# Performance work log

Hardware: AMD Instinct MI355X
Metric: run time of the kernel (lower is better)

The kernel has to match this reference:

```python
import jax, jax.numpy as jnp
import numpy as np

B, F, V, D_EMB = 16384, 32, 50000, 16
D_IN = F * D_EMB            # 512, concat embedding dim
N_TASK, N_SPEC, N_SH = 2, 2, 2
E = N_TASK * N_SPEC + N_SH  # 6 experts per CGC level
H1, H2 = 512, 256           # expert_params dims
T1, T2 = 128, 64            # tower dims


def setup_inputs() -> dict:
    key = jax.random.key(0)
    ks = iter(jax.random.split(key, 32))
    def w(shape, s=0.05):
        return jax.random.normal(next(ks), shape, jnp.float32) * s
    return dict(
        x_ids=jax.random.randint(next(ks), (B, F), 0, V),
        emb=w((F, V, D_EMB)),
        e1_W1=w((E, D_IN, H1)), e1_b1=jnp.zeros((E, H1), jnp.float32),
        e1_W2=w((E, H1, H2)), e1_b2=jnp.zeros((E, H2), jnp.float32),
        g1_Ws=w((N_TASK, D_IN, N_SPEC + N_SH)), g1_bs=jnp.zeros((N_TASK, N_SPEC + N_SH), jnp.float32),
        g1_Wsh=w((D_IN, E)), g1_bsh=jnp.zeros((E,), jnp.float32),
        e2_W1=w((E, H2, H1)), e2_b1=jnp.zeros((E, H1), jnp.float32),
        e2_W2=w((E, H1, H2)), e2_b2=jnp.zeros((E, H2), jnp.float32),
        g2_Ws=w((N_TASK, H2, N_SPEC + N_SH)), g2_bs=jnp.zeros((N_TASK, N_SPEC + N_SH), jnp.float32),
        tw_W1=w((N_TASK, H2, T1)), tw_b1=jnp.zeros((N_TASK, T1), jnp.float32),
        tw_W2=w((N_TASK, T1, T2)), tw_b2=jnp.zeros((N_TASK, T2), jnp.float32),
    )


def _cgc(x_list, W1, b1, W2, b2, Wg, bg, Wg_sh=None, bg_sh=None):
    # Stack expert inputs: task-t specific experts read x_list[t], shared read x_list[-1].
    X = jnp.stack([x_list[0]] * N_SPEC + [x_list[1]] * N_SPEC + [x_list[-1]] * N_SH)  # [E,B,Din]
    # Grouped two-layer expert MLP (BatchNorm is identity at eval-mode init).
    h = jax.nn.relu(jnp.einsum('ebd,edh->ebh', X, W1) + b1[:, None, :])   # [E,B,H1]
    out = jax.nn.relu(jnp.einsum('ebh,eho->ebo', h, W2) + b2[:, None, :])  # [E,B,H2]
    outs = []
    for t in range(N_TASK):
        gate = jax.nn.softmax(x_list[t] @ Wg[t] + bg[t], axis=-1)          # [B, N_SPEC+N_SH]
        sel = jnp.concatenate([out[t * N_SPEC:(t + 1) * N_SPEC], out[-N_SH:]], axis=0)
        outs.append(jnp.einsum('bk,kbo->bo', gate, sel))
    if Wg_sh is not None:  # shared gate only for levels < n_level
        gate = jax.nn.softmax(x_list[-1] @ Wg_sh + bg_sh, axis=-1)          # [B,E]
        outs.append(jnp.einsum('bk,kbo->bo', gate, out))
    return outs


def reference(x_ids, emb, e1_W1, e1_b1, e1_W2, e1_b2, g1_Ws, g1_bs, g1_Wsh, g1_bsh,
              e2_W1, e2_b1, e2_W2, e2_b2, g2_Ws, g2_bs, tw_W1, tw_b1, tw_W2, tw_b2):
    # Embedding lookup per sparse feature, then flatten (squeeze_dim=True).
    embed_x = emb[jnp.arange(F)[None, :], x_ids].reshape(B, D_IN)  # [B, 512]
    xs = [embed_x] * (N_TASK + 1)
    xs = _cgc(xs, e1_W1, e1_b1, e1_W2, e1_b2, g1_Ws, g1_bs, g1_Wsh, g1_bsh)  # level 1 -> 3 outs
    xs = _cgc(xs, e2_W1, e2_b1, e2_W2, e2_b2, g2_Ws, g2_bs)                  # level 2 -> 2 outs
    ys = []
    for t in range(N_TASK):
        h = jax.nn.relu(xs[t] @ tw_W1[t] + tw_b1[t])
        h = jax.nn.relu(h @ tw_W2[t] + tw_b2[t])
        ys.append(jax.nn.sigmoid(h))  # PredictionLayer('classification')
    return jnp.concatenate(ys, axis=1)  # [B, N_TASK*T2]
```

## Files before the change

### kernel.cpp

```cpp
#include <hip/hip_runtime.h>

typedef unsigned short u16;
typedef __attribute__((ext_vector_type(4))) unsigned short u16x4;
typedef __attribute__((ext_vector_type(8))) unsigned short u16x8;
typedef __attribute__((ext_vector_type(8))) short s16x8;
typedef __attribute__((ext_vector_type(4))) float f32x4;

#define BATCH 16384
#define NFEAT 32
#define NVOCAB 50000

__device__ __forceinline__ u16 f2bf(float f) {
    union { float f; unsigned u; } v; v.f = f;
    unsigned u = v.u;
    return (u16)((u + 0x7fffu + ((u >> 16) & 1u)) >> 16);
}
__device__ __forceinline__ float bf2f(u16 h) {
    union { unsigned u; float f; } v; v.u = ((unsigned)h) << 16;
    return v.f;
}

__device__ __forceinline__ void load_lds16(const u16* g, u16* l) {
    __builtin_amdgcn_global_load_lds(
        (const __attribute__((address_space(1))) void*)g,
        (__attribute__((address_space(3))) void*)l, 16, 0, 0);
}

struct PrepDesc { const float* src; u16* dst; int K; int N; int nz; int zbase; };
struct PrepArgs { PrepDesc d[6]; };

__global__ void prep_weights(PrepArgs args) {
    int z = blockIdx.z;
    int di = 0;
    #pragma unroll
    for (int i = 0; i < 6; i++)
        if (z >= args.d[i].zbase && z < args.d[i].zbase + args.d[i].nz) di = i;
    PrepDesc d = args.d[di];
    int zz = z - d.zbase;
    int k0 = blockIdx.x * 32, n0 = blockIdx.y * 32;
    if (k0 >= d.K || n0 >= d.N) return;
    __shared__ float tile[32][33];
    const float* src = d.src + (long)zz * d.K * d.N;
    u16* dst = d.dst + (long)zz * d.K * d.N;
    int tx = threadIdx.x & 31, ty = threadIdx.x >> 5;
    for (int r = ty; r < 32; r += 8) {
        int k = k0 + r, n = n0 + tx;
        tile[r][tx] = (k < d.K && n < d.N) ? src[(long)k * d.N + n] : 0.f;
    }
    __syncthreads();
    for (int r = ty; r < 32; r += 8) {
        int n = n0 + r, k = k0 + tx;
        if (n < d.N && k < d.K) dst[(long)n * d.K + k] = f2bf(tile[tx][r]);
    }
}

__global__ void gather_embed(const int* __restrict__ ids,
                             const float* __restrict__ emb,
                             u16* __restrict__ out) {
    int idx = blockIdx.x * 256 + threadIdx.x;
    int d4 = idx & 3;
    int f  = (idx >> 2) & 31;
    int b  = idx >> 7;
    int id = ids[b * NFEAT + f];
    const float4* p = (const float4*)(emb + ((long)f * NVOCAB + id) * 16) + d4;
    float4 v = *p;
    u16x4 o;
    o.x = f2bf(v.x); o.y = f2bf(v.y); o.z = f2bf(v.z); o.w = f2bf(v.w);
    *(u16x4*)(out + (long)b * 512 + f * 16 + d4 * 4) = o;
}

struct GemmP {
    const u16* A; const u16* Bt; const float* bias; u16* C;
    int N, K, a_zshift, c_row_stride; long a_zstride, c_zstride;
};

__device__ __forceinline__ void gemm_impl(const GemmP p) {
    __shared__ u16 sA[128 * 64];
    __shared__ u16 sB[256 * 64];
    const int z = blockIdx.z;
    const u16* Ab = p.A + (long)(z >> p.a_zshift) * p.a_zstride;
    const u16* Bb = p.Bt + (long)z * p.N * p.K;
    const int m0 = blockIdx.x * 128;
    const int n0 = blockIdx.y * 256;
    const int tid = threadIdx.x;
    const int lane = tid & 63;
    const int w = tid >> 6;
    const int wm = (w & 1) * 64;
    const int wn = (w >> 1) * 128;
    const int l16 = lane & 15;
    const int q = lane >> 4;
    const int key = l16 & 7;
    const int K = p.K;

    const int tr = tid >> 3;
    const int lc = (tid & 7) ^ (tr & 7);
    const u16* gA0 = Ab + (long)(m0 + tr) * K + lc * 8;
    const u16* gB0 = Bb + (long)(n0 + tr) * K + lc * 8;
    u16* lA0 = &sA[(tid & ~63) * 8];
    u16* lB0 = &sB[(tid & ~63) * 8];

    f32x4 acc[4][8] = {};

    for (int k0 = 0; k0 < K; k0 += 64) {
        if (k0) __syncthreads();
        #pragma unroll
        for (int i = 0; i < 4; i++)
            load_lds16(gA0 + (long)(32 * i) * K + k0, lA0 + i * 256 * 8);
        #pragma unroll
        for (int i = 0; i < 8; i++)
            load_lds16(gB0 + (long)(32 * i) * K + k0, lB0 + i * 256 * 8);
        __syncthreads();
        #pragma unroll
        for (int kk = 0; kk < 2; kk++) {
            const int pc = ((kk << 2) | q) ^ key;
            s16x8 af[4], bf[8];
            #pragma unroll
            for (int mt = 0; mt < 4; mt++)
                af[mt] = *(const s16x8*)(&sA[(wm + mt * 16 + l16) * 64 + pc * 8]);
            #pragma unroll
            for (int nt = 0; nt < 8; nt++)
                bf[nt] = *(const s16x8*)(&sB[(wn + nt * 16 + l16) * 64 + pc * 8]);
            #pragma unroll
            for (int mt = 0; mt < 4; mt++)
                #pragma unroll
                for (int nt = 0; nt < 8; nt++)
                    acc[mt][nt] = __builtin_amdgcn_mfma_f32_16x16x32_bf16(
                        bf[nt], af[mt], acc[mt][nt], 0, 0, 0);
        }
    }

    const float* bb = p.bias + (long)z * p.N;
    u16* Cp = p.C + (long)z * p.c_zstride;
    #pragma unroll
    for (int mt = 0; mt < 4; mt++) {
        int grow = m0 + wm + mt * 16 + l16;
        u16* rowp = Cp + (long)grow * p.c_row_stride;
        #pragma unroll
        for (int nt = 0; nt < 8; nt++) {
            int gc = n0 + wn + nt * 16 + q * 4;
            float4 bv = *(const float4*)(bb + gc);
            f32x4 v = acc[mt][nt];
            v.x = fmaxf(v.x + bv.x, 0.f);
            v.y = fmaxf(v.y + bv.y, 0.f);
            v.z = fmaxf(v.z + bv.z, 0.f);
            v.w = fmaxf(v.w + bv.w, 0.f);
            u16x4 o;
            o.x = f2bf(v.x); o.y = f2bf(v.y); o.z = f2bf(v.z); o.w = f2bf(v.w);
            *(u16x4*)(rowp + gc) = o;
        }
    }
}

__global__ __launch_bounds__(256, 2) void gemm_l1a(GemmP p) { gemm_impl(p); }
__global__ __launch_bounds__(256, 2) void gemm_l1b(GemmP p) { gemm_impl(p); }
__global__ __launch_bounds__(256, 2) void gemm_l2a(GemmP p) { gemm_impl(p); }
__global__ __launch_bounds__(256, 2) void gemm_l2b(GemmP p) { gemm_impl(p); }

__global__ __launch_bounds__(256, 1)
void tower_fused(const u16* __restrict__ x2, const u16* __restrict__ W1t,
                 const float* __restrict__ b1, const u16* __restrict__ W2t,
                 const float* __restrict__ b2, float* __restrict__ out) {
    const int t = blockIdx.y, m0 = blockIdx.x * 64;
    __shared__ u16 sX[64 * 256];
    __shared__ u16 sW1[128 * 256];
    __shared__ u16 sH[64 * 136];
    __shared__ u16 sW2[64 * 128];
    __shared__ float sB1[128];
    __shared__ float sB2[64];
    const int tid = threadIdx.x, lane = tid & 63, w = tid >> 6;
    const int l16 = lane & 15, q = lane >> 4;

    #pragma unroll
    for (int i = 0; i < 8; i++) {
        int c = i * 256 + tid, row = c >> 5, kc = c & 31;
        int lcc = (kc & ~7) | ((kc & 7) ^ (row & 7));
        load_lds16(x2 + ((long)t * BATCH + m0 + row) * 256 + lcc * 8,
                   &sX[(i * 256 + (tid & ~63)) * 8]);
    }
    #pragma unroll
    for (int i = 0; i < 16; i++) {
        int c = i * 256 + tid, row = c >> 5, kc = c & 31;
        int lcc = (kc & ~7) | ((kc & 7) ^ (row & 7));
        load_lds16(W1t + ((long)t * 128 + row) * 256 + lcc * 8,
                   &sW1[(i * 256 + (tid & ~63)) * 8]);
    }
    #pragma unroll
    for (int i = 0; i < 4; i++) {
        int c = i * 256 + tid, row = c >> 4, kc = c & 15;
        int lcc = (kc & ~7) | ((kc & 7) ^ (row & 7));
        load_lds16(W2t + ((long)t * 64 + row) * 128 + lcc * 8,
                   &sW2[(i * 256 + (tid & ~63)) * 8]);
    }
    if (tid < 128) sB1[tid] = b1[t * 128 + tid];
    if (tid < 64)  sB2[tid] = b2[t * 64 + tid];
    __syncthreads();

    f32x4 acc1[4][2] = {};
    #pragma unroll
    for (int kk = 0; kk < 8; kk++) {
        int pcb = kk * 4 + q;
        s16x8 af[4], bf[2];
        #pragma unroll
        for (int mt = 0; mt < 4; mt++) {
            int row = mt * 16 + l16;
            int sc = (pcb & ~7) | ((pcb & 7) ^ (row & 7));
            af[mt] = *(const s16x8*)(&sX[row * 256 + sc * 8]);
        }
        #pragma unroll
        for (int nt = 0; nt < 2; nt++) {
            int row = w * 32 + nt * 16 + l16;
            int sc = (pcb & ~7) | ((pcb & 7) ^ (row & 7));
            bf[nt] = *(const s16x8*)(&sW1[row * 256 + sc * 8]);
        }
        #pragma unroll
        for (int mt = 0; mt < 4; mt++)
            #pragma unroll
            for (int nt = 0; nt < 2; nt++)
                acc1[mt][nt] = __builtin_amdgcn_mfma_f32_16x16x32_bf16(
                    bf[nt], af[mt], acc1[mt][nt], 0, 0, 0);
    }
    #pragma unroll
    for (int mt = 0; mt < 4; mt++) {
        int row = mt * 16 + l16;
        #pragma unroll
        for (int nt = 0; nt < 2; nt++) {
            int col = w * 32 + nt * 16 + q * 4;
            f32x4 v = acc1[mt][nt];
            u16x4 o;
            o.x = f2bf(fmaxf(v.x + sB1[col + 0], 0.f));
            o.y = f2bf(fmaxf(v.y + sB1[col + 1], 0.f));
            o.z = f2bf(fmaxf(v.z + sB1[col + 2], 0.f));
            o.w = f2bf(fmaxf(v.w + sB1[col + 3], 0.f));
            *(u16x4*)(&sH[row * 136 + col]) = o;
        }
    }
    __syncthreads();

    f32x4 acc2[4] = {};
    #pragma unroll
    for (int kk = 0; kk < 4; kk++) {
        s16x8 af[4], bf;
        #pragma unroll
        for (int mt = 0; mt < 4; mt++) {
            int row = mt * 16 + l16;
            af[mt] = *(const s16x8*)(&sH[row * 136 + kk * 32 + q * 8]);
        }
        {
            int row = w * 16 + l16;
            int pc = kk * 4 + q;
            int sc = (pc & ~7) | ((pc & 7) ^ (row & 7));
            bf = *(const s16x8*)(&sW2[row * 128 + sc * 8]);
        }
        #pragma unroll
        for (int mt = 0; mt < 4; mt++)
            acc2[mt] = __builtin_amdgcn_mfma_f32_16x16x32_bf16(
                bf, af[mt], acc2[mt], 0, 0, 0);
    }
    #pragma unroll
    for (int mt = 0; mt < 4; mt++) {
        int grow = m0 + mt * 16 + l16;
        int col = w * 16 + q * 4;
        float4 bv = *(const float4*)(sB2 + col);
        f32x4 v = acc2[mt];
        float4 r;
        r.x = 1.f / (1.f + __expf(-(v.x + bv.x)));
        r.y = 1.f / (1.f + __expf(-(v.y + bv.y)));
        r.z = 1.f / (1.f + __expf(-(v.z + bv.z)));
        r.w = 1.f / (1.f + __expf(-(v.w + bv.w)));
        *(float4*)(out + (long)grow * 128 + t * 64 + col) = r;
    }
}

__global__ __launch_bounds__(256)
void gate1(const u16* __restrict__ embed, const u16* __restrict__ out1,
           const float* __restrict__ g1Ws, const float* __restrict__ g1bs,
           const float* __restrict__ gWsh, const float* __restrict__ gbsh,
           u16* __restrict__ x1) {
    const int m0 = blockIdx.x * 8;
    __shared__ float sg[8][16];
    const int tid = threadIdx.x;
    const int row = tid >> 5, l = tid & 31;
    const long rb = m0 + row;

    float a[4] = {0,0,0,0}, b[4] = {0,0,0,0}, c[6] = {0,0,0,0,0,0};
    {
        const u16* er = embed + rb * 512 + l * 16;
        u16x8 xa = *(const u16x8*)(er);
        u16x8 xb = *(const u16x8*)(er + 8);
        #pragma unroll
        for (int u = 0; u < 16; u++) {
            int k = l * 16 + u;
            float xv = bf2f(u < 8 ? xa[u] : xb[u - 8]);
            float4 wa = *(const float4*)(g1Ws + k * 4);
            float4 wb = *(const float4*)(g1Ws + 2048 + k * 4);
            a[0] += xv * wa.x; a[1] += xv * wa.y; a[2] += xv * wa.z; a[3] += xv * wa.w;
            b[0] += xv * wb.x; b[1] += xv * wb.y; b[2] += xv * wb.z; b[3] += xv * wb.w;
            float2 w0 = *(const float2*)(gWsh + k * 6);
            float2 w1 = *(const float2*)(gWsh + k * 6 + 2);
            float2 w2 = *(const float2*)(gWsh + k * 6 + 4);
            c[0] += xv * w0.x; c[1] += xv * w0.y;
            c[2] += xv * w1.x; c[3] += xv * w1.y;
            c[4] += xv * w2.x; c[5] += xv * w2.y;
        }
    }
    #pragma unroll
    for (int off = 1; off < 32; off <<= 1) {
        #pragma unroll
        for (int g = 0; g < 4; g++) { a[g] += __shfl_xor(a[g], off); b[g] += __shfl_xor(b[g], off); }
        #pragma unroll
        for (int g = 0; g < 6; g++) c[g] += __shfl_xor(c[g], off);
    }
    if (l == 0) {
        float mx, s, e[6];
        mx = -1e30f;
        for (int g = 0; g < 4; g++) { a[g] += g1bs[g]; mx = fmaxf(mx, a[g]); }
        s = 0.f; for (int g = 0; g < 4; g++) { e[g] = __expf(a[g] - mx); s += e[g]; }
        for (int g = 0; g < 4; g++) sg[row][g] = e[g] / s;
        mx = -1e30f;
        for (int g = 0; g < 4; g++) { b[g] += g1bs[4 + g]; mx = fmaxf(mx, b[g]); }
        s = 0.f; for (int g = 0; g < 4; g++) { e[g] = __expf(b[g] - mx); s += e[g]; }
        for (int g = 0; g < 4; g++) sg[row][4 + g] = e[g] / s;
        mx = -1e30f;
        for (int g = 0; g < 6; g++) { c[g] += gbsh[g]; mx = fmaxf(mx, c[g]); }
        s = 0.f; for (int g = 0; g < 6; g++) { e[g] = __expf(c[g] - mx); s += e[g]; }
        for (int g = 0; g < 6; g++) sg[row][8 + g] = e[g] / s;
    }
    __syncthreads();

    const int c8 = l * 8;
    const u16* ob = out1 + rb * 256 + c8;
    u16x8 o[6];
    #pragma unroll
    for (int k = 0; k < 6; k++) o[k] = *(const u16x8*)(ob + (long)k * BATCH * 256);
    const float* g = sg[row];
    u16x8 r0, r1, r2;
    #pragma unroll
    for (int u = 0; u < 8; u++) {
        float o0 = bf2f(o[0][u]), o1 = bf2f(o[1][u]), o2 = bf2f(o[2][u]);
        float o3 = bf2f(o[3][u]), o4 = bf2f(o[4][u]), o5 = bf2f(o[5][u]);
        r0[u] = f2bf(g[0] * o0 + g[1] * o1 + g[2] * o4 + g[3] * o5);
        r1[u] = f2bf(g[4] * o2 + g[5] * o3 + g[6] * o4 + g[7] * o5);
        r2[u] = f2bf(g[8] * o0 + g[9] * o1 + g[10] * o2 + g[11] * o3 + g[12] * o4 + g[13] * o5);
    }
    *(u16x8*)(x1 + ((long)0 * BATCH + rb) * 256 + c8) = r0;
    *(u16x8*)(x1 + ((long)1 * BATCH + rb) * 256 + c8) = r1;
    *(u16x8*)(x1 + ((long)2 * BATCH + rb) * 256 + c8) = r2;
}

__global__ __launch_bounds__(256)
void gate2(const u16* __restrict__ x1, const u16* __restrict__ out2,
           const float* __restrict__ g2Ws, const float* __restrict__ g2bs,
           u16* __restrict__ x2) {
    const int m0 = blockIdx.x * 8;
    __shared__ float sg[8][8];
    const int tid = threadIdx.x;
    const int row = tid >> 5, l = tid & 31;
    const long rb = m0 + row;

    float a[4] = {0,0,0,0}, b[4] = {0,0,0,0};
    {
        const u16* e0 = x1 + rb * 256 + l * 8;
        const u16* e1 = e0 + (long)BATCH * 256;
        u16x8 x0 = *(const u16x8*)e0;
        u16x8 x1v = *(const u16x8*)e1;
        #pragma unroll
        for (int u = 0; u < 8; u++) {
            int k = l * 8 + u;
            float4 wa = *(const float4*)(g2Ws + k * 4);
            float4 wb = *(const float4*)(g2Ws + 1024 + k * 4);
            float xv0 = bf2f(x0[u]), xv1 = bf2f(x1v[u]);
            a[0] += xv0 * wa.x; a[1] += xv0 * wa.y; a[2] += xv0 * wa.z; a[3] += xv0 * wa.w;
            b[0] += xv1 * wb.x; b[1] += xv1 * wb.y; b[2] += xv1 * wb.z; b[3] += xv1 * wb.w;
        }
    }
    #pragma unroll
    for (int off = 1; off < 32; off <<= 1) {
        #pragma unroll
        for (int g = 0; g < 4; g++) { a[g] += __shfl_xor(a[g], off); b[g] += __shfl_xor(b[g], off); }
    }
    if (l == 0) {
        float mx, s, e[4];
        mx = -1e30f;
        for (int g = 0; g < 4; g++) { a[g] += g2bs[g]; mx = fmaxf(mx, a[g]); }
        s = 0.f; for (int g = 0; g < 4; g++) { e[g] = __expf(a[g] - mx); s += e[g]; }
        for (int g = 0; g < 4; g++) sg[row][g] = e[g] / s;
        mx = -1e30f;
        for (int g = 0; g < 4; g++) { b[g] += g2bs[4 + g]; mx = fmaxf(mx, b[g]); }
        s = 0.f; for (int g = 0; g < 4; g++) { e[g] = __expf(b[g] - mx); s += e[g]; }
        for (int g = 0; g < 4; g++) sg[row][4 + g] = e[g] / s;
    }
    __syncthreads();

    const int c8 = l * 8;
    const u16* ob = out2 + rb * 256 + c8;
    u16x8 o[6];
    #pragma unroll
    for (int k = 0; k < 6; k++) o[k] = *(const u16x8*)(ob + (long)k * BATCH * 256);
    const float* g = sg[row];
    u16x8 r0, r1;
    #pragma unroll
    for (int u = 0; u < 8; u++) {
        float o0 = bf2f(o[0][u]), o1 = bf2f(o[1][u]), o2 = bf2f(o[2][u]);
        float o3 = bf2f(o[3][u]), o4 = bf2f(o[4][u]), o5 = bf2f(o[5][u]);
        r0[u] = f2bf(g[0] * o0 + g[1] * o1 + g[2] * o4 + g[3] * o5);
        r1[u] = f2bf(g[4] * o2 + g[5] * o3 + g[6] * o4 + g[7] * o5);
    }
    *(u16x8*)(x2 + ((long)0 * BATCH + rb) * 256 + c8) = r0;
    *(u16x8*)(x2 + ((long)1 * BATCH + rb) * 256 + c8) = r1;
}

extern "C" void kernel_launch(void* const* d_in, const int* in_sizes, int n_in,
                              void* d_out, int out_size, void* d_ws, size_t ws_size,
                              hipStream_t stream) {
    const int*   x_ids = (const int*)  d_in[0];
    const float* emb   = (const float*)d_in[1];
    const float* e1W1  = (const float*)d_in[2];
    const float* e1b1  = (const float*)d_in[3];
    const float* e1W2  = (const float*)d_in[4];
    const float* e1b2  = (const float*)d_in[5];
    const float* g1Ws  = (const float*)d_in[6];
    const float* g1bs  = (const float*)d_in[7];
    const float* g1Wsh = (const float*)d_in[8];
    const float* g1bsh = (const float*)d_in[9];
    const float* e2W1  = (const float*)d_in[10];
    const float* e2b1  = (const float*)d_in[11];
    const float* e2W2  = (const float*)d_in[12];
    const float* e2b2  = (const float*)d_in[13];
    const float* g2Ws  = (const float*)d_in[14];
    const float* g2bs  = (const float*)d_in[15];
    const float* twW1  = (const float*)d_in[16];
    const float* twb1  = (const float*)d_in[17];
    const float* twW2  = (const float*)d_in[18];
    const float* twb2  = (const float*)d_in[19];
    float* out = (float*)d_out;

    char* ws = (char*)d_ws;
    u16* embed   = (u16*)(ws + 0);
    u16* wt_e1W1 = (u16*)(ws + 16777216);
    u16* wt_e1W2 = (u16*)(ws + 19922944);
    u16* wt_e2W1 = (u16*)(ws + 21495808);
    u16* wt_e2W2 = (u16*)(ws + 23068672);
    u16* wt_twW1 = (u16*)(ws + 24641536);
    u16* wt_twW2 = (u16*)(ws + 24772608);
    u16* h_buf   = (u16*)(ws + 24805376);
    u16* o_buf   = (u16*)(ws + 125468672);
    u16* x1      = (u16*)(ws + 175800320);
    u16* x2      = (u16*)(ws + 200966144);

    PrepArgs pa;
    pa.d[0] = { e1W1, wt_e1W1, 512, 512, 6,  0 };
    pa.d[1] = { e1W2, wt_e1W2, 512, 256, 6,  6 };
    pa.d[2] = { e2W1, wt_e2W1, 256, 512, 6, 12 };
    pa.d[3] = { e2W2, wt_e2W2, 512, 256, 6, 18 };
    pa.d[4] = { twW1, wt_twW1, 256, 128, 2, 24 };
    pa.d[5] = { twW2, wt_twW2, 128,  64, 2, 26 };
    prep_weights<<<dim3(16, 16, 28), 256, 0, stream>>>(pa);

    gather_embed<<<dim3(BATCH * NFEAT * 4 / 256), 256, 0, stream>>>(x_ids, emb, embed);

    GemmP p1a = { embed, wt_e1W1, e1b1, h_buf, 512, 512, 0, 512, 0L, (long)BATCH * 512 };
    gemm_l1a<<<dim3(128, 2, 6), 256, 0, stream>>>(p1a);

    GemmP p1b = { h_buf, wt_e1W2, e1b2, o_buf, 256, 512, 0, 256,
                  (long)BATCH * 512, (long)BATCH * 256 };
    gemm_l1b<<<dim3(128, 1, 6), 256, 0, stream>>>(p1b);

    gate1<<<dim3(BATCH / 8), 256, 0, stream>>>(embed, o_buf, g1Ws, g1bs, g1Wsh, g1bsh, x1);

    GemmP p2a = { x1, wt_e2W1, e2b1, h_buf, 512, 256, 1, 512,
                  (long)BATCH * 256, (long)BATCH * 512 };
    gemm_l2a<<<dim3(128, 2, 6), 256, 0, stream>>>(p2a);

    GemmP p2b = { h_buf, wt_e2W2, e2b2, o_buf, 256, 512, 0, 256,
                  (long)BATCH * 512, (long)BATCH * 256 };
    gemm_l2b<<<dim3(128, 1, 6), 256, 0, stream>>>(p2b);

    gate2<<<dim3(BATCH / 8), 256, 0, stream>>>(x1, o_buf, g2Ws, g2bs, x2);

    tower_fused<<<dim3(BATCH / 64, 2), 256, 0, stream>>>(x2, wt_twW1, twb1, wt_twW2, twb2, out);
}
```

Baseline: 522.7 us.

## Fuse all stages into one persistent kernel with software grid barriers

Replaces the nine separate kernel launches (weight prep, gather, four GEMMs, two gates, tower) with a single persistent kernel of 512 blocks. The stages are separated by an atomic-counter grid barrier, and GEMM tiles are distributed round-robin over the blocks. Weight prep and the embedding gather now run concurrently on disjoint block subsets. This is meant to remove per-launch overhead and inter-kernel gaps, at the cost of barrier spin time and a fixed block count that depends on every block being co-resident. The tower now reads weights from global memory instead of staging them in LDS.

```diff
diff --git a/kernel.cpp b/kernel.cpp
--- a/kernel.cpp
+++ b/kernel.cpp
@@ -9,6 +9,7 @@
 #define BATCH 16384
 #define NFEAT 32
 #define NVOCAB 50000
+#define NBLK 512
 
 __device__ __forceinline__ u16 f2bf(float f) {
     union { float f; unsigned u; } v; v.f = f;
@@ -19,69 +20,51 @@
     union { unsigned u; float f; } v; v.u = ((unsigned)h) << 16;
     return v.f;
 }
-
 __device__ __forceinline__ void load_lds16(const u16* g, u16* l) {
     __builtin_amdgcn_global_load_lds(
         (const __attribute__((address_space(1))) void*)g,
         (__attribute__((address_space(3))) void*)l, 16, 0, 0);
 }
 
-struct PrepDesc { const float* src; u16* dst; int K; int N; int nz; int zbase; };
-struct PrepArgs { PrepDesc d[6]; };
-
-__global__ void prep_weights(PrepArgs args) {
-    int z = blockIdx.z;
-    int di = 0;
-    #pragma unroll
-    for (int i = 0; i < 6; i++)
-        if (z >= args.d[i].zbase && z < args.d[i].zbase + args.d[i].nz) di = i;
-    PrepDesc d = args.d[di];
-    int zz = z - d.zbase;
-    int k0 = blockIdx.x * 32, n0 = blockIdx.y * 32;
-    if (k0 >= d.K || n0 >= d.N) return;
-    __shared__ float tile[32][33];
-    const float* src = d.src + (long)zz * d.K * d.N;
-    u16* dst = d.dst + (long)zz * d.K * d.N;
-    int tx = threadIdx.x & 31, ty = threadIdx.x >> 5;
-    for (int r = ty; r < 32; r += 8) {
-        int k = k0 + r, n = n0 + tx;
-        tile[r][tx] = (k < d.K && n < d.N) ? src[(long)k * d.N + n] : 0.f;
-    }
+__device__ __forceinline__ void grid_sync(unsigned* cnt, unsigned* gen) {
     __syncthreads();
-    for (int r = ty; r < 32; r += 8) {
-        int n = n0 + r, k = k0 + tx;
-        if (n < d.N && k < d.K) dst[(long)n * d.K + k] = f2bf(tile[tx][r]);
-    }
-}
-
-__global__ void gather_embed(const int* __restrict__ ids,
-                             const float* __restrict__ emb,
-                             u16* __restrict__ out) {
-    int idx = blockIdx.x * 256 + threadIdx.x;
-    int d4 = idx & 3;
-    int f  = (idx >> 2) & 31;
-    int b  = idx >> 7;
-    int id = ids[b * NFEAT + f];
-    const float4* p = (const float4*)(emb + ((long)f * NVOCAB + id) * 16) + d4;
-    float4 v = *p;
-    u16x4 o;
-    o.x = f2bf(v.x); o.y = f2bf(v.y); o.z = f2bf(v.z); o.w = f2bf(v.w);
-    *(u16x4*)(out + (long)b * 512 + f * 16 + d4 * 4) = o;
-}
-
-struct GemmP {
-    const u16* A; const u16* Bt; const float* bias; u16* C;
-    int N, K, a_zshift, c_row_stride; long a_zstride, c_zstride;
+    if (threadIdx.x == 0) {
+        __threadfence();
+        unsigned arrival = __hip_atomic_fetch_add(cnt, 1u, __ATOMIC_ACQ_REL,
+                                                  __HIP_MEMORY_SCOPE_AGENT) + 1u;
+        unsigned target = (arrival + NBLK - 1u) / NBLK;
+        if (arrival % NBLK == 0u)
+            __hip_atomic_fetch_add(gen, 1u, __ATOMIC_ACQ_REL,
+                                   __HIP_MEMORY_SCOPE_AGENT);
+        while (__hip_atomic_load(gen, __ATOMIC_ACQUIRE,
+                                 __HIP_MEMORY_SCOPE_AGENT) < target)
+            __builtin_amdgcn_s_sleep(1);
+        __threadfence();
+    }
+    __syncthreads();
+}
+
+struct MonoArgs {
+    const int* x_ids; const float* emb;
+    const float* e1W1; const float* e1b1; const float* e1W2; const float* e1b2;
+    const float* g1Ws; const float* g1bs; const float* g1Wsh; const float* g1bsh;
+    const float* e2W1; const float* e2b1; const float* e2W2; const float* e2b2;
+    const float* g2Ws; const float* g2bs;
+    const float* twW1; const float* twb1; const float* twW2; const float* twb2;
+    u16* embed; u16* wt_e1W1; u16* wt_e1W2; u16* wt_e2W1; u16* wt_e2W2;
+    u16* wt_twW1; u16* wt_twW2; u16* h_buf; u16* o_buf; u16* x1; u16* x2;
+    unsigned* bar;
+    float* out;
 };
 
-__device__ __forceinline__ void gemm_impl(const GemmP p) {
-    __shared__ u16 sA[128 * 64];
-    __shared__ u16 sB[256 * 64];
-    const int z = blockIdx.z;
-    const u16* Ab = p.A + (long)(z >> p.a_zshift) * p.a_zstride;
-    const u16* Bb = p.Bt + (long)z * p.N * p.K;
-    const int m0 = blockIdx.x * 128;
-    const int n0 = blockIdx.y * 256;
+__device__ __forceinline__ void gemm_core(const u16* __restrict__ Ab,
+                                          const u16* __restrict__ Bb,
+                                          const float* __restrict__ bb,
+                                          u16* __restrict__ Cp,
+                                          int N, int K, int m0, int n0,
+                                          char* smem) {
+    u16* sA = (u16*)smem;
+    u16* sB = (u16*)(smem + 16384);
     const int tid = threadIdx.x;
     const int lane = tid & 63;
     const int w = tid >> 6;
@@ -90,7 +73,6 @@
     const int l16 = lane & 15;
     const int q = lane >> 4;
     const int key = l16 & 7;
-    const int K = p.K;
 
     const int tr = tid >> 3;
     const int lc = (tid & 7) ^ (tr & 7);
@@ -129,12 +111,10 @@
         }
     }
 
-    const float* bb = p.bias + (long)z * p.N;
-    u16* Cp = p.C + (long)z * p.c_zstride;
     #pragma unroll
     for (int mt = 0; mt < 4; mt++) {
         int grow = m0 + wm + mt * 16 + l16;
-        u16* rowp = Cp + (long)grow * p.c_row_stride;
+        u16* rowp = Cp + (long)grow * N;
         #pragma unroll
         for (int nt = 0; nt < 8; nt++) {
             int gc = n0 + wn + nt * 16 + q * 4;
@@ -151,331 +131,357 @@
     }
 }
 
-__global__ __launch_bounds__(256, 2) void gemm_l1a(GemmP p) { gemm_impl(p); }
-__global__ __launch_bounds__(256, 2) void gemm_l1b(GemmP p) { gemm_impl(p); }
-__global__ __launch_bounds__(256, 2) void gemm_l2a(GemmP p) { gemm_impl(p); }
-__global__ __launch_bounds__(256, 2) void gemm_l2b(GemmP p) { gemm_impl(p); }
-
-__global__ __launch_bounds__(256, 1)
-void tower_fused(const u16* __restrict__ x2, const u16* __restrict__ W1t,
-                 const float* __restrict__ b1, const u16* __restrict__ W2t,
-                 const float* __restrict__ b2, float* __restrict__ out) {
-    const int t = blockIdx.y, m0 = blockIdx.x * 64;
-    __shared__ u16 sX[64 * 256];
-    __shared__ u16 sW1[128 * 256];
-    __shared__ u16 sH[64 * 136];
-    __shared__ u16 sW2[64 * 128];
-    __shared__ float sB1[128];
-    __shared__ float sB2[64];
-    const int tid = threadIdx.x, lane = tid & 63, w = tid >> 6;
+__device__ void gemm_phase(const u16* A, long a_zstride, int a_zshift,
+                           const u16* Bt, const float* bias, u16* C,
+                           int N, int K, char* smem) {
+    const int ny = N >> 8;
+    const int per_m = ny * 6;
+    const int njobs = 128 * per_m;
+    for (int job = blockIdx.x; job < njobs; job += NBLK) {
+        int m0 = (job / per_m) * 128;
+        int rem = job % per_m;
+        int z = rem / ny;
+        int n0 = (rem % ny) * 256;
+        __syncthreads();
+        gemm_core(A + (long)(z >> a_zshift) * a_zstride,
+                  Bt + (long)z * N * K,
+                  bias + (long)z * N,
+                  C + (long)z * BATCH * N,
+                  N, K, m0, n0, smem);
+    }
+}
+
+__global__ __launch_bounds__(256, 2)
+void mono(MonoArgs a) {
+    __shared__ __align__(16) char smem[49152];
+    unsigned* bcnt = a.bar;
+    unsigned* bgen = a.bar + 16;
+    const int tid = threadIdx.x;
+    const int lane = tid & 63, w4 = tid >> 6;
     const int l16 = lane & 15, q = lane >> 4;
 
-    #pragma unroll
-    for (int i = 0; i < 8; i++) {
-        int c = i * 256 + tid, row = c >> 5, kc = c & 31;
-        int lcc = (kc & ~7) | ((kc & 7) ^ (row & 7));
-        load_lds16(x2 + ((long)t * BATCH + m0 + row) * 256 + lcc * 8,
-                   &sX[(i * 256 + (tid & ~63)) * 8]);
-    }
-    #pragma unroll
-    for (int i = 0; i < 16; i++) {
-        int c = i * 256 + tid, row = c >> 5, kc = c & 31;
-        int lcc = (kc & ~7) | ((kc & 7) ^ (row & 7));
-        load_lds16(W1t + ((long)t * 128 + row) * 256 + lcc * 8,
-                   &sW1[(i * 256 + (tid & ~63)) * 8]);
-    }
-    #pragma unroll
-    for (int i = 0; i < 4; i++) {
-        int c = i * 256 + tid, row = c >> 4, kc = c & 15;
-        int lcc = (kc & ~7) | ((kc & 7) ^ (row & 7));
-        load_lds16(W2t + ((long)t * 64 + row) * 128 + lcc * 8,
-                   &sW2[(i * 256 + (tid & ~63)) * 8]);
-    }
-    if (tid < 128) sB1[tid] = b1[t * 128 + tid];
-    if (tid < 64)  sB2[tid] = b2[t * 64 + tid];
-    __syncthreads();
-
-    f32x4 acc1[4][2] = {};
-    #pragma unroll
-    for (int kk = 0; kk < 8; kk++) {
-        int pcb = kk * 4 + q;
-        s16x8 af[4], bf[2];
-        #pragma unroll
-        for (int mt = 0; mt < 4; mt++) {
-            int row = mt * 16 + l16;
-            int sc = (pcb & ~7) | ((pcb & 7) ^ (row & 7));
-            af[mt] = *(const s16x8*)(&sX[row * 256 + sc * 8]);
-        }
-        #pragma unroll
-        for (int nt = 0; nt < 2; nt++) {
-            int row = w * 32 + nt * 16 + l16;
-            int sc = (pcb & ~7) | ((pcb & 7) ^ (row & 7));
-            bf[nt] = *(const s16x8*)(&sW1[row * 256 + sc * 8]);
-        }
-        #pragma unroll
-        for (int mt = 0; mt < 4; mt++)
-            #pragma unroll
-            for (int nt = 0; nt < 2; nt++)
-                acc1[mt][nt] = __builtin_amdgcn_mfma_f32_16x16x32_bf16(
-                    bf[nt], af[mt], acc1[mt][nt], 0, 0, 0);
-    }
-    #pragma unroll
-    for (int mt = 0; mt < 4; mt++) {
-        int row = mt * 16 + l16;
-        #pragma unroll
-        for (int nt = 0; nt < 2; nt++) {
-            int col = w * 32 + nt * 16 + q * 4;
-            f32x4 v = acc1[mt][nt];
+    if (blockIdx.x < 256) {
+        for (long idx = (long)blockIdx.x * 256 + tid; idx < (long)BATCH * NFEAT * 4;
+             idx += 65536) {
+            int d4 = (int)(idx & 3);
+            int f  = (int)((idx >> 2) & 31);
+            int b  = (int)(idx >> 7);
+            int id = a.x_ids[b * NFEAT + f];
+            float4 v = *((const float4*)(a.emb + ((long)f * NVOCAB + id) * 16) + d4);
             u16x4 o;
-            o.x = f2bf(fmaxf(v.x + sB1[col + 0], 0.f));
-            o.y = f2bf(fmaxf(v.y + sB1[col + 1], 0.f));
-            o.z = f2bf(fmaxf(v.z + sB1[col + 2], 0.f));
-            o.w = f2bf(fmaxf(v.w + sB1[col + 3], 0.f));
-            *(u16x4*)(&sH[row * 136 + col]) = o;
-        }
-    }
-    __syncthreads();
-
-    f32x4 acc2[4] = {};
-    #pragma unroll
-    for (int kk = 0; kk < 4; kk++) {
-        s16x8 af[4], bf;
-        #pragma unroll
-        for (int mt = 0; mt < 4; mt++) {
-            int row = mt * 16 + l16;
-            af[mt] = *(const s16x8*)(&sH[row * 136 + kk * 32 + q * 8]);
-        }
-        {
-            int row = w * 16 + l16;
-            int pc = kk * 4 + q;
-            int sc = (pc & ~7) | ((pc & 7) ^ (row & 7));
-            bf = *(const s16x8*)(&sW2[row * 128 + sc * 8]);
-        }
-        #pragma unroll
-        for (int mt = 0; mt < 4; mt++)
-            acc2[mt] = __builtin_amdgcn_mfma_f32_16x16x32_bf16(
-                bf, af[mt], acc2[mt], 0, 0, 0);
-    }
-    #pragma unroll
-    for (int mt = 0; mt < 4; mt++) {
-        int grow = m0 + mt * 16 + l16;
-        int col = w * 16 + q * 4;
-        float4 bv = *(const float4*)(sB2 + col);
-        f32x4 v = acc2[mt];
-        float4 r;
-        r.x = 1.f / (1.f + __expf(-(v.x + bv.x)));
-        r.y = 1.f / (1.f + __expf(-(v.y + bv.y)));
-        r.z = 1.f / (1.f + __expf(-(v.z + bv.z)));
-        r.w = 1.f / (1.f + __expf(-(v.w + bv.w)));
-        *(float4*)(out + (long)grow * 128 + t * 64 + col) = r;
-    }
-}
-
-__global__ __launch_bounds__(256)
-void gate1(const u16* __restrict__ embed, const u16* __restrict__ out1,
-           const float* __restrict__ g1Ws, const float* __restrict__ g1bs,
-           const float* __restrict__ gWsh, const float* __restrict__ gbsh,
-           u16* __restrict__ x1) {
-    const int m0 = blockIdx.x * 8;
-    __shared__ float sg[8][16];
-    const int tid = threadIdx.x;
-    const int row = tid >> 5, l = tid & 31;
-    const long rb = m0 + row;
-
-    float a[4] = {0,0,0,0}, b[4] = {0,0,0,0}, c[6] = {0,0,0,0,0,0};
+            o.x = f2bf(v.x); o.y = f2bf(v.y); o.z = f2bf(v.z); o.w = f2bf(v.w);
+            *(u16x4*)(a.embed + (long)b * 512 + f * 16 + d4 * 4) = o;
+        }
+    } else {
+        float* tile = (float*)smem;
+        const int tx = tid & 31, ty = tid >> 5;
+        for (int j = blockIdx.x - 256; j < 7168; j += 256) {
+            int z = j >> 8;
+            int rem = j & 255;
+            const float* src; u16* dst; int K, N, zb;
+            if      (z <  6) { src = a.e1W1; dst = a.wt_e1W1; K = 512; N = 512; zb = 0; }
+            else if (z < 12) { src = a.e1W2; dst = a.wt_e1W2; K = 512; N = 256; zb = 6; }
+            else if (z < 18) { src = a.e2W1; dst = a.wt_e2W1; K = 256; N = 512; zb = 12; }
+            else if (z < 24) { src = a.e2W2; dst = a.wt_e2W2; K = 512; N = 256; zb = 18; }
+            else if (z < 26) { src = a.twW1; dst = a.wt_twW1; K = 256; N = 128; zb = 24; }
+            else             { src = a.twW2; dst = a.wt_twW2; K = 128; N = 64;  zb = 26; }
+            int zz = z - zb;
+            int k0 = (rem & 15) * 32, n0 = (rem >> 4) * 32;
+            if (k0 >= K || n0 >= N) continue;
+            __syncthreads();
+            const float* s = src + (long)zz * K * N;
+            u16* d = dst + (long)zz * K * N;
+            for (int r = ty; r < 32; r += 8) {
+                int k = k0 + r, n = n0 + tx;
+                tile[r * 33 + tx] = (k < K && n < N) ? s[(long)k * N + n] : 0.f;
+            }
+            __syncthreads();
+            for (int r = ty; r < 32; r += 8) {
+                int n = n0 + r, k = k0 + tx;
+                if (n < N && k < K) d[(long)n * K + k] = f2bf(tile[tx * 33 + r]);
+            }
+        }
+    }
+    grid_sync(bcnt, bgen);
+
+    gemm_phase(a.embed, 0L, 3, a.wt_e1W1, a.e1b1, a.h_buf, 512, 512, smem);
+    grid_sync(bcnt, bgen);
+
+    gemm_phase(a.h_buf, (long)BATCH * 512, 0, a.wt_e1W2, a.e1b2, a.o_buf, 256, 512, smem);
+    grid_sync(bcnt, bgen);
+
     {
-        const u16* er = embed + rb * 512 + l * 16;
-        u16x8 xa = *(const u16x8*)(er);
-        u16x8 xb = *(const u16x8*)(er + 8);
-        #pragma unroll
-        for (int u = 0; u < 16; u++) {
-            int k = l * 16 + u;
-            float xv = bf2f(u < 8 ? xa[u] : xb[u - 8]);
-            float4 wa = *(const float4*)(g1Ws + k * 4);
-            float4 wb = *(const float4*)(g1Ws + 2048 + k * 4);
-            a[0] += xv * wa.x; a[1] += xv * wa.y; a[2] += xv * wa.z; a[3] += xv * wa.w;
-            b[0] += xv * wb.x; b[1] += xv * wb.y; b[2] += xv * wb.z; b[3] += xv * wb.w;
-            float2 w0 = *(const float2*)(gWsh + k * 6);
-            float2 w1 = *(const float2*)(gWsh + k * 6 + 2);
-            float2 w2 = *(const float2*)(gWsh + k * 6 + 4);
-            c[0] += xv * w0.x; c[1] += xv * w0.y;
-            c[2] += xv * w1.x; c[3] += xv * w1.y;
-            c[4] += xv * w2.x; c[5] += xv * w2.y;
-        }
-    }
-    #pragma unroll
-    for (int off = 1; off < 32; off <<= 1) {
-        #pragma unroll
-        for (int g = 0; g < 4; g++) { a[g] += __shfl_xor(a[g], off); b[g] += __shfl_xor(b[g], off); }
-        #pragma unroll
-        for (int g = 0; g < 6; g++) c[g] += __shfl_xor(c[g], off);
-    }
-    if (l == 0) {
-        float mx, s, e[6];
-        mx = -1e30f;
-        for (int g = 0; g < 4; g++) { a[g] += g1bs[g]; mx = fmaxf(mx, a[g]); }
-        s = 0.f; for (int g = 0; g < 4; g++) { e[g] = __expf(a[g] - mx); s += e[g]; }
-        for (int g = 0; g < 4; g++) sg[row][g] = e[g] / s;
-        mx = -1e30f;
-        for (int g = 0; g < 4; g++) { b[g] += g1bs[4 + g]; mx = fmaxf(mx, b[g]); }
-        s = 0.f; for (int g = 0; g < 4; g++) { e[g] = __expf(b[g] - mx); s += e[g]; }
-        for (int g = 0; g < 4; g++) sg[row][4 + g] = e[g] / s;
-        mx = -1e30f;
-        for (int g = 0; g < 6; g++) { c[g] += gbsh[g]; mx = fmaxf(mx, c[g]); }
-        s = 0.f; for (int g = 0; g < 6; g++) { e[g] = __expf(c[g] - mx); s += e[g]; }
-        for (int g = 0; g < 6; g++) sg[row][8 + g] = e[g] / s;
-    }
-    __syncthreads();
-
-    const int c8 = l * 8;
-    const u16* ob = out1 + rb * 256 + c8;
-    u16x8 o[6];
-    #pragma unroll
-    for (int k = 0; k < 6; k++) o[k] = *(const u16x8*)(ob + (long)k * BATCH * 256);
-    const float* g = sg[row];
-    u16x8 r0, r1, r2;
-    #pragma unroll
-    for (int u = 0; u < 8; u++) {
-        float o0 = bf2f(o[0][u]), o1 = bf2f(o[1][u]), o2 = bf2f(o[2][u]);
-        float o3 = bf2f(o[3][u]), o4 = bf2f(o[4][u]), o5 = bf2f(o[5][u]);
-        r0[u] = f2bf(g[0] * o0 + g[1] * o1 + g[2] * o4 + g[3] * o5);
-        r1[u] = f2bf(g[4] * o2 + g[5] * o3 + g[6] * o4 + g[7] * o5);
-        r2[u] = f2bf(g[8] * o0 + g[9] * o1 + g[10] * o2 + g[11] * o3 + g[12] * o4 + g[13] * o5);
-    }
-    *(u16x8*)(x1 + ((long)0 * BATCH + rb) * 256 + c8) = r0;
-    *(u16x8*)(x1 + ((long)1 * BATCH + rb) * 256 + c8) = r1;
-    *(u16x8*)(x1 + ((long)2 * BATCH + rb) * 256 + c8) = r2;
-}
-
-__global__ __launch_bounds__(256)
-void gate2(const u16* __restrict__ x1, const u16* __restrict__ out2,
-           const float* __restrict__ g2Ws, const float* __restrict__ g2bs,
-           u16* __restrict__ x2) {
-    const int m0 = blockIdx.x * 8;
-    __shared__ float sg[8][8];
-    const int tid = threadIdx.x;
-    const int row = tid >> 5, l = tid & 31;
-    const long rb = m0 + row;
-
-    float a[4] = {0,0,0,0}, b[4] = {0,0,0,0};
+        float (*sg)[16] = (float(*)[16])smem;
+        const int row = tid >> 5, l = tid & 31;
+        for (int job = blockIdx.x; job < 2048; job += NBLK) {
+            const long rb = (long)job * 8 + row;
+            float ga[4] = {0,0,0,0}, gb[4] = {0,0,0,0}, gc[6] = {0,0,0,0,0,0};
+            {
+                const u16* er = a.embed + rb * 512 + l * 16;
+                u16x8 xa = *(const u16x8*)(er);
+                u16x8 xb = *(const u16x8*)(er + 8);
+                #pragma unroll
+                for (int u = 0; u < 16; u++) {
+                    int k = l * 16 + u;
+                    float xv = bf2f(u < 8 ? xa[u] : xb[u - 8]);
+                    float4 wa = *(const float4*)(a.g1Ws + k * 4);
+                    float4 wb = *(const float4*)(a.g1Ws + 2048 + k * 4);
+                    ga[0] += xv * wa.x; ga[1] += xv * wa.y; ga[2] += xv * wa.z; ga[3] += xv * wa.w;
+                    gb[0] += xv * wb.x; gb[1] += xv * wb.y; gb[2] += xv * wb.z; gb[3] += xv * wb.w;
+                    float2 w0 = *(const float2*)(a.g1Wsh + k * 6);
+                    float2 w1 = *(const float2*)(a.g1Wsh + k * 6 + 2);
+                    float2 w2 = *(const float2*)(a.g1Wsh + k * 6 + 4);
+                    gc[0] += xv * w0.x; gc[1] += xv * w0.y;
+                    gc[2] += xv * w1.x; gc[3] += xv * w1.y;
+                    gc[4] += xv * w2.x; gc[5] += xv * w2.y;
+                }
+            }
+            #pragma unroll
+            for (int off = 1; off < 32; off <<= 1) {
+                #pragma unroll
+                for (int g = 0; g < 4; g++) { ga[g] += __shfl_xor(ga[g], off); gb[g] += __shfl_xor(gb[g], off); }
+                #pragma unroll
+                for (int g = 0; g < 6; g++) gc[g] += __shfl_xor(gc[g], off);
+            }
+            if (l == 0) {
+                float mx, s, e[6];
+                mx = -1e30f;
+                for (int g = 0; g < 4; g++) { ga[g] += a.g1bs[g]; mx = fmaxf(mx, ga[g]); }
+                s = 0.f; for (int g = 0; g < 4; g++) { e[g] = __expf(ga[g] - mx); s += e[g]; }
+                for (int g = 0; g < 4; g++) sg[row][g] = e[g] / s;
+                mx = -1e30f;
+                for (int g = 0; g < 4; g++) { gb[g] += a.g1bs[4 + g]; mx = fmaxf(mx, gb[g]); }
+                s = 0.f; for (int g = 0; g < 4; g++) { e[g] = __expf(gb[g] - mx); s += e[g]; }
+                for (int g = 0; g < 4; g++) sg[row][4 + g] = e[g] / s;
+                mx = -1e30f;
+                for (int g = 0; g < 6; g++) { gc[g] += a.g1bsh[g]; mx = fmaxf(mx, gc[g]); }
+                s = 0.f; for (int g = 0; g < 6; g++) { e[g] = __expf(gc[g] - mx); s += e[g]; }
+                for (int g = 0; g < 6; g++) sg[row][8 + g] = e[g] / s;
+            }
+            __syncthreads();
+            const int c8 = l * 8;
+            const u16* ob = a.o_buf + rb * 256 + c8;
+            u16x8 o[6];
+            #pragma unroll
+            for (int k = 0; k < 6; k++) o[k] = *(const u16x8*)(ob + (long)k * BATCH * 256);
+            const float* g = sg[row];
+            u16x8 r0, r1, r2;
+            #pragma unroll
+            for (int u = 0; u < 8; u++) {
+                float o0 = bf2f(o[0][u]), o1 = bf2f(o[1][u]), o2 = bf2f(o[2][u]);
+                float o3 = bf2f(o[3][u]), o4 = bf2f(o[4][u]), o5 = bf2f(o[5][u]);
+                r0[u] = f2bf(g[0] * o0 + g[1] * o1 + g[2] * o4 + g[3] * o5);
+                r1[u] = f2bf(g[4] * o2 + g[5] * o3 + g[6] * o4 + g[7] * o5);
+                r2[u] = f2bf(g[8] * o0 + g[9] * o1 + g[10] * o2 + g[11] * o3 + g[12] * o4 + g[13] * o5);
+            }
+            *(u16x8*)(a.x1 + ((long)0 * BATCH + rb) * 256 + c8) = r0;
+            *(u16x8*)(a.x1 + ((long)1 * BATCH + rb) * 256 + c8) = r1;
+            *(u16x8*)(a.x1 + ((long)2 * BATCH + rb) * 256 + c8) = r2;
+            __syncthreads();
+        }
+    }
+    grid_sync(bcnt, bgen);
+
+    gemm_phase(a.x1, (long)BATCH * 256, 1, a.wt_e2W1, a.e2b1, a.h_buf, 512, 256, smem);
+    grid_sync(bcnt, bgen);
+
+    gemm_phase(a.h_buf, (long)BATCH * 512, 0, a.wt_e2W2, a.e2b2, a.o_buf, 256, 512, smem);
+    grid_sync(bcnt, bgen);
+
     {
-        const u16* e0 = x1 + rb * 256 + l * 8;
-        const u16* e1 = e0 + (long)BATCH * 256;
-        u16x8 x0 = *(const u16x8*)e0;
-        u16x8 x1v = *(const u16x8*)e1;
-        #pragma unroll
-        for (int u = 0; u < 8; u++) {
-            int k = l * 8 + u;
-            float4 wa = *(const float4*)(g2Ws + k * 4);
-            float4 wb = *(const float4*)(g2Ws + 1024 + k * 4);
-            float xv0 = bf2f(x0[u]), xv1 = bf2f(x1v[u]);
-            a[0] += xv0 * wa.x; a[1] += xv0 * wa.y; a[2] += xv0 * wa.z; a[3] += xv0 * wa.w;
-            b[0] += xv1 * wb.x; b[1] += xv1 * wb.y; b[2] += xv1 * wb.z; b[3] += xv1 * wb.w;
-        }
-    }
-    #pragma unroll
-    for (int off = 1; off < 32; off <<= 1) {
-        #pragma unroll
-        for (int g = 0; g < 4; g++) { a[g] += __shfl_xor(a[g], off); b[g] += __shfl_xor(b[g], off); }
-    }
-    if (l == 0) {
-        float mx, s, e[4];
-        mx = -1e30f;
-        for (int g = 0; g < 4; g++) { a[g] += g2bs[g]; mx = fmaxf(mx, a[g]); }
-        s = 0.f; for (int g = 0; g < 4; g++) { e[g] = __expf(a[g] - mx); s += e[g]; }
-        for (int g = 0; g < 4; g++) sg[row][g] = e[g] / s;
-        mx = -1e30f;
-        for (int g = 0; g < 4; g++) { b[g] += g2bs[4 + g]; mx = fmaxf(mx, b[g]); }
-        s = 0.f; for (int g = 0; g < 4; g++) { e[g] = __expf(b[g] - mx); s += e[g]; }
-        for (int g = 0; g < 4; g++) sg[row][4 + g] = e[g] / s;
-    }
-    __syncthreads();
-
-    const int c8 = l * 8;
-    const u16* ob = out2 + rb * 256 + c8;
-    u16x8 o[6];
-    #pragma unroll
-    for (int k = 0; k < 6; k++) o[k] = *(const u16x8*)(ob + (long)k * BATCH * 256);
-    const float* g = sg[row];
-    u16x8 r0, r1;
-    #pragma unroll
-    for (int u = 0; u < 8; u++) {
-        float o0 = bf2f(o[0][u]), o1 = bf2f(o[1][u]), o2 = bf2f(o[2][u]);
-        float o3 = bf2f(o[3][u]), o4 = bf2f(o[4][u]), o5 = bf2f(o[5][u]);
-        r0[u] = f2bf(g[0] * o0 + g[1] * o1 + g[2] * o4 + g[3] * o5);
-        r1[u] = f2bf(g[4] * o2 + g[5] * o3 + g[6] * o4 + g[7] * o5);
-    }
-    *(u16x8*)(x2 + ((long)0 * BATCH + rb) * 256 + c8) = r0;
-    *(u16x8*)(x2 + ((long)1 * BATCH + rb) * 256 + c8) = r1;
+        float (*sg)[8] = (float(*)[8])smem;
+        const int row = tid >> 5, l = tid & 31;
+        for (int job = blockIdx.x; job < 2048; job += NBLK) {
+            const long rb = (long)job * 8 + row;
+            float ga[4] = {0,0,0,0}, gb[4] = {0,0,0,0};
+            {
+                const u16* e0 = a.x1 + rb * 256 + l * 8;
+                const u16* e1 = e0 + (long)BATCH * 256;
+                u16x8 x0 = *(const u16x8*)e0;
+                u16x8 x1v = *(const u16x8*)e1;
+                #pragma unroll
+                for (int u = 0; u < 8; u++) {
+                    int k = l * 8 + u;
+                    float4 wa = *(const float4*)(a.g2Ws + k * 4);
+                    float4 wb = *(const float4*)(a.g2Ws + 1024 + k * 4);
+                    float xv0 = bf2f(x0[u]), xv1 = bf2f(x1v[u]);
+                    ga[0] += xv0 * wa.x; ga[1] += xv0 * wa.y; ga[2] += xv0 * wa.z; ga[3] += xv0 * wa.w;
+                    gb[0] += xv1 * wb.x; gb[1] += xv1 * wb.y; gb[2] += xv1 * wb.z; gb[3] += xv1 * wb.w;
+                }
+            }
+            #pragma unroll
+            for (int off = 1; off < 32; off <<= 1) {
+                #pragma unroll
+                for (int g = 0; g < 4; g++) { ga[g] += __shfl_xor(ga[g], off); gb[g] += __shfl_xor(gb[g], off); }
+            }
+            if (l == 0) {
+                float mx, s, e[4];
+                mx = -1e30f;
+                for (int g = 0; g < 4; g++) { ga[g] += a.g2bs[g]; mx = fmaxf(mx, ga[g]); }
+                s = 0.f; for (int g = 0; g < 4; g++) { e[g] = __expf(ga[g] - mx); s += e[g]; }
+                for (int g = 0; g < 4; g++) sg[row][g] = e[g] / s;
+                mx = -1e30f;
+                for (int g = 0; g < 4; g++) { gb[g] += a.g2bs[4 + g]; mx = fmaxf(mx, gb[g]); }
+                s = 0.f; for (int g = 0; g < 4; g++) { e[g] = __expf(gb[g] - mx); s += e[g]; }
+                for (int g = 0; g < 4; g++) sg[row][4 + g] = e[g] / s;
+            }
+            __syncthreads();
+            const int c8 = l * 8;
+            const u16* ob = a.o_buf + rb * 256 + c8;
+            u16x8 o[6];
+            #pragma unroll
+            for (int k = 0; k < 6; k++) o[k] = *(const u16x8*)(ob + (long)k * BATCH * 256);
+            const float* g = sg[row];
+            u16x8 r0, r1;
+            #pragma unroll
+            for (int u = 0; u < 8; u++) {
+                float o0 = bf2f(o[0][u]), o1 = bf2f(o[1][u]), o2 = bf2f(o[2][u]);
+                float o3 = bf2f(o[3][u]), o4 = bf2f(o[4][u]), o5 = bf2f(o[5][u]);
+                r0[u] = f2bf(g[0] * o0 + g[1] * o1 + g[2] * o4 + g[3] * o5);
+                r1[u] = f2bf(g[4] * o2 + g[5] * o3 + g[6] * o4 + g[7] * o5);
+            }
+            *(u16x8*)(a.x2 + ((long)0 * BATCH + rb) * 256 + c8) = r0;
+            *(u16x8*)(a.x2 + ((long)1 * BATCH + rb) * 256 + c8) = r1;
+            __syncthreads();
+        }
+    }
+    grid_sync(bcnt, bgen);
+
+    {
+        u16* sX = (u16*)smem;
+        u16* sH = (u16*)(smem + 32768);
+        for (int job = blockIdx.x; job < 512; job += NBLK) {
+            int t = job >> 8;
+            int m0 = (job & 255) * 64;
+            const u16* W1 = a.wt_twW1 + (long)t * 128 * 256;
+            const u16* W2 = a.wt_twW2 + (long)t * 64 * 128;
+            __syncthreads();
+            #pragma unroll
+            for (int i = 0; i < 8; i++) {
+                int p = i * 256 + tid, row = p >> 5, pcc = p & 31;
+                int c = (pcc & ~7) | ((pcc & 7) ^ (row & 7));
+                load_lds16(a.x2 + ((long)t * BATCH + m0 + row) * 256 + c * 8,
+                           sX + (i * 256 + (tid & ~63)) * 8);
+            }
+            __syncthreads();
+            f32x4 acc1[4][2] = {};
+            #pragma unroll
+            for (int kk = 0; kk < 8; kk++) {
+                s16x8 af[4], bf[2];
+                #pragma unroll
+                for (int nt = 0; nt < 2; nt++) {
+                    int nrow = w4 * 32 + nt * 16 + l16;
+                    bf[nt] = *(const s16x8*)(W1 + (long)nrow * 256 + kk * 32 + q * 8);
+                }
+                #pragma unroll
+                for (int mt = 0; mt < 4; mt++) {
+                    int row = mt * 16 + l16;
+                    int cc = kk * 4 + q;
+                    int pc = (cc & ~7) | ((cc & 7) ^ (row & 7));
+                    af[mt] = *(const s16x8*)(&sX[row * 256 + pc * 8]);
+                }
+                #pragma unroll
+                for (int mt = 0; mt < 4; mt++)
+                    #pragma unroll
+                    for (int nt = 0; nt < 2; nt++)
+                        acc1[mt][nt] = __builtin_amdgcn_mfma_f32_16x16x32_bf16(
+                            bf[nt], af[mt], acc1[mt][nt], 0, 0, 0);
+            }
+            #pragma unroll
+            for (int mt = 0; mt < 4; mt++) {
+                int row = mt * 16 + l16;
+                #pragma unroll
+                for (int nt = 0; nt < 2; nt++) {
+                    int col = w4 * 32 + nt * 16 + q * 4;
+                    float4 bv = *(const float4*)(a.twb1 + t * 128 + col);
+                    f32x4 v = acc1[mt][nt];
+                    u16x4 o;
+                    o.x = f2bf(fmaxf(v.x + bv.x, 0.f));
+                    o.y = f2bf(fmaxf(v.y + bv.y, 0.f));
+                    o.z = f2bf(fmaxf(v.z + bv.z, 0.f));
+                    o.w = f2bf(fmaxf(v.w + bv.w, 0.f));
+                    int c = col >> 3;
+                    int pc = (c & ~7) | ((c & 7) ^ (row & 7));
+                    *(u16x4*)(&sH[row * 128 + pc * 8 + (col & 7)]) = o;
+                }
+            }
+            __syncthreads();
+            f32x4 acc2[4] = {};
+            #pragma unroll
+            for (int kk = 0; kk < 4; kk++) {
+                s16x8 af[4], bfv;
+                {
+                    int nrow = w4 * 16 + l16;
+                    bfv = *(const s16x8*)(W2 + (long)nrow * 128 + kk * 32 + q * 8);
+                }
+                #pragma unroll
+                for (int mt = 0; mt < 4; mt++) {
+                    int row = mt * 16 + l16;
+                    int cc = kk * 4 + q;
+                    int pc = (cc & ~7) | ((cc & 7) ^ (row & 7));
+                    af[mt] = *(const s16x8*)(&sH[row * 128 + pc * 8]);
+                }
+                #pragma unroll
+                for (int mt = 0; mt < 4; mt++)
+                    acc2[mt] = __builtin_amdgcn_mfma_f32_16x16x32_bf16(
+                        bfv, af[mt], acc2[mt], 0, 0, 0);
+            }
+            #pragma unroll
+            for (int mt = 0; mt < 4; mt++) {
+                int grow = m0 + mt * 16 + l16;
+                int col = w4 * 16 + q * 4;
+                float4 bv = *(const float4*)(a.twb2 + t * 64 + col);
+                f32x4 v = acc2[mt];
+                float4 r;
+                r.x = 1.f / (1.f + __expf(-(v.x + bv.x)));
+                r.y = 1.f / (1.f + __expf(-(v.y + bv.y)));
+                r.z = 1.f / (1.f + __expf(-(v.z + bv.z)));
+                r.w = 1.f / (1.f + __expf(-(v.w + bv.w)));
+                *(float4*)(a.out + (long)grow * 128 + t * 64 + col) = r;
+            }
+        }
+    }
 }
 
 extern "C" void kernel_launch(void* const* d_in, const int* in_sizes, int n_in,
                               void* d_out, int out_size, void* d_ws, size_t ws_size,
                               hipStream_t stream) {
-    const int*   x_ids = (const int*)  d_in[0];
-    const float* emb   = (const float*)d_in[1];
-    const float* e1W1  = (const float*)d_in[2];
-    const float* e1b1  = (const float*)d_in[3];
-    const float* e1W2  = (const float*)d_in[4];
-    const float* e1b2  = (const float*)d_in[5];
-    const float* g1Ws  = (const float*)d_in[6];
-    const float* g1bs  = (const float*)d_in[7];
-    const float* g1Wsh = (const float*)d_in[8];
-    const float* g1bsh = (const float*)d_in[9];
-    const float* e2W1  = (const float*)d_in[10];
-    const float* e2b1  = (const float*)d_in[11];
-    const float* e2W2  = (const float*)d_in[12];
-    const float* e2b2  = (const float*)d_in[13];
-    const float* g2Ws  = (const float*)d_in[14];
-    const float* g2bs  = (const float*)d_in[15];
-    const float* twW1  = (const float*)d_in[16];
-    const float* twb1  = (const float*)d_in[17];
-    const float* twW2  = (const float*)d_in[18];
-    const float* twb2  = (const float*)d_in[19];
-    float* out = (float*)d_out;
-
     char* ws = (char*)d_ws;
-    u16* embed   = (u16*)(ws + 0);
-    u16* wt_e1W1 = (u16*)(ws + 16777216);
-    u16* wt_e1W2 = (u16*)(ws + 19922944);
-    u16* wt_e2W1 = (u16*)(ws + 21495808);
-    u16* wt_e2W2 = (u16*)(ws + 23068672);
-    u16* wt_twW1 = (u16*)(ws + 24641536);
-    u16* wt_twW2 = (u16*)(ws + 24772608);
-    u16* h_buf   = (u16*)(ws + 24805376);
-    u16* o_buf   = (u16*)(ws + 125468672);
-    u16* x1      = (u16*)(ws + 175800320);
-    u16* x2      = (u16*)(ws + 200966144);
-
-    PrepArgs pa;
-    pa.d[0] = { e1W1, wt_e1W1, 512, 512, 6,  0 };
-    pa.d[1] = { e1W2, wt_e1W2, 512, 256, 6,  6 };
-    pa.d[2] = { e2W1, wt_e2W1, 256, 512, 6, 12 };
-    pa.d[3] = { e2W2, wt_e2W2, 512, 256, 6, 18 };
-    pa.d[4] = { twW1, wt_twW1, 256, 128, 2, 24 };
-    pa.d[5] = { twW2, wt_twW2, 128,  64, 2, 26 };
-    prep_weights<<<dim3(16, 16, 28), 256, 0, stream>>>(pa);
-
-    gather_embed<<<dim3(BATCH * NFEAT * 4 / 256), 256, 0, stream>>>(x_ids, emb, embed);
-
-    GemmP p1a = { embed, wt_e1W1, e1b1, h_buf, 512, 512, 0, 512, 0L, (long)BATCH * 512 };
-    gemm_l1a<<<dim3(128, 2, 6), 256, 0, stream>>>(p1a);
-
-    GemmP p1b = { h_buf, wt_e1W2, e1b2, o_buf, 256, 512, 0, 256,
-                  (long)BATCH * 512, (long)BATCH * 256 };
-    gemm_l1b<<<dim3(128, 1, 6), 256, 0, stream>>>(p1b);
-
-    gate1<<<dim3(BATCH / 8), 256, 0, stream>>>(embed, o_buf, g1Ws, g1bs, g1Wsh, g1bsh, x1);
-
-    GemmP p2a = { x1, wt_e2W1, e2b1, h_buf, 512, 256, 1, 512,
-                  (long)BATCH * 256, (long)BATCH * 512 };
-    gemm_l2a<<<dim3(128, 2, 6), 256, 0, stream>>>(p2a);
-
-    GemmP p2b = { h_buf, wt_e2W2, e2b2, o_buf, 256, 512, 0, 256,
-                  (long)BATCH * 512, (long)BATCH * 256 };
-    gemm_l2b<<<dim3(128, 1, 6), 256, 0, stream>>>(p2b);
-
-    gate2<<<dim3(BATCH / 8), 256, 0, stream>>>(x1, o_buf, g2Ws, g2bs, x2);
-
-    tower_fused<<<dim3(BATCH / 64, 2), 256, 0, stream>>>(x2, wt_twW1, twb1, wt_twW2, twb2, out);
-}
+    MonoArgs a;
+    a.x_ids = (const int*)  d_in[0];
+    a.emb   = (const float*)d_in[1];
+    a.e1W1  = (const float*)d_in[2];
+    a.e1b1  = (const float*)d_in[3];
+    a.e1W2  = (const float*)d_in[4];
+    a.e1b2  = (const float*)d_in[5];
+    a.g1Ws  = (const float*)d_in[6];
+    a.g1bs  = (const float*)d_in[7];
+    a.g1Wsh = (const float*)d_in[8];
+    a.g1bsh = (const float*)d_in[9];
+    a.e2W1  = (const float*)d_in[10];
+    a.e2b1  = (const float*)d_in[11];
+    a.e2W2  = (const float*)d_in[12];
+    a.e2b2  = (const float*)d_in[13];
+    a.g2Ws  = (const float*)d_in[14];
+    a.g2bs  = (const float*)d_in[15];
+    a.twW1  = (const float*)d_in[16];
+    a.twb1  = (const float*)d_in[17];
+    a.twW2  = (const float*)d_in[18];
+    a.twb2  = (const float*)d_in[19];
+    a.embed   = (u16*)(ws + 0);
+    a.wt_e1W1 = (u16*)(ws + 16777216);
+    a.wt_e1W2 = (u16*)(ws + 19922944);
+    a.wt_e2W1 = (u16*)(ws + 21495808);
+    a.wt_e2W2 = (u16*)(ws + 23068672);
+    a.wt_twW1 = (u16*)(ws + 24641536);
+    a.wt_twW2 = (u16*)(ws + 24772608);
+    a.h_buf   = (u16*)(ws + 24805376);
+    a.o_buf   = (u16*)(ws + 125468672);
+    a.x1      = (u16*)(ws + 175800320);
+    a.x2      = (u16*)(ws + 200966144);
+    a.bar     = (unsigned*)(ws + 218103808);
+    a.out     = (float*)d_out;
+
+    hipMemsetAsync((void*)a.bar, 0, 128, stream);
+    mono<<<dim3(NBLK), dim3(256), 0, stream>>>(a);
+}
```

After: 1.611 ms. 208% more time.
